# Kernel tuning notes

Hardware: AMD Instinct MI355X
Metric: run time of the kernel (lower is better)

Reference implementation:

```python
import jax, jax.numpy as jnp
import numpy as np


def setup_inputs() -> dict:
    key = jax.random.key(0)
    kx, ks = jax.random.split(key)
    X = jax.random.normal(kx, (8, 4096, 16), dtype=jnp.float32)
    # nn.Parameter(torch.rand(1) + 1.0)
    sigma = jax.random.uniform(ks, (1,), dtype=jnp.float32) + 1.0
    return {"X": X, "sigma": sigma}


def reference(X, sigma):
    sq = jnp.sum(X * X, axis=-1)                       # [B, N]
    inner = jnp.einsum('bnf,bmf->bnm', X, X)           # [B, N, N]
    sqdist = sq[:, :, None] + sq[:, None, :] - 2.0 * inner
    sqdist = jnp.maximum(sqdist, 0.0)                  # guard tiny negatives
    gaussian = jnp.exp(-sqdist / sigma[0])             # [B, N, N]
    # original _softmax: exp(gaussian) / sum over dim 2 == softmax over axis 2
    return jax.nn.softmax(gaussian, axis=2)
```

## Files before the change

### kernel.cpp

```cpp
#include <hip/hip_runtime.h>


constexpr int Bn  = 8;
constexpr int N   = 4096;
constexpr int F   = 16;
constexpr int TN  = 4;
constexpr int BLK = 512;
constexpr int WPB = BLK / 64;
constexpr int ITERS = N / (BLK * 4);

__global__ __launch_bounds__(256)
void pack_kernel(const float* __restrict__ X, float* __restrict__ Xt) {
    const int b = blockIdx.y;
    const int m = blockIdx.x * 256 + threadIdx.x;
    const float4* src = (const float4*)(X + ((size_t)b * N + m) * F);
    const float4 v0 = src[0], v1 = src[1], v2 = src[2], v3 = src[3];
    const float x[F] = {v0.x, v0.y, v0.z, v0.w, v1.x, v1.y, v1.z, v1.w,
                        v2.x, v2.y, v2.z, v2.w, v3.x, v3.y, v3.z, v3.w};
    float* dst = Xt + (size_t)b * F * N + m;
    #pragma unroll
    for (int f = 0; f < F; ++f) dst[(size_t)f * N] = x[f];
}

__device__ __forceinline__ float dot4(float4 a, float4 b) {
    return fmaf(a.x, b.x, fmaf(a.y, b.y, fmaf(a.z, b.z, a.w * b.w)));
}

__device__ __forceinline__ float gse(float d, float base, float nis) {
    float sqd = fmaxf(fmaf(-2.0f, d, base), 0.0f);
    return __expf(__expf(sqd * nis));
}

__global__ __launch_bounds__(BLK, 4)
void gs_main(const float* __restrict__ X, const float* __restrict__ Xt,
             const float* __restrict__ sigma_p, float* __restrict__ out) {
    __shared__ float lds_e[TN][N];
    __shared__ float red[TN][WPB];

    const int tid = threadIdx.x;
    const int b   = blockIdx.y;
    const int n0  = blockIdx.x * TN;
    const float* Xb = X + (size_t)b * N * F;

    float4 q0[TN], q1[TN], q2[TN], q3[TN];
    float  sqn[TN];
    #pragma unroll
    for (int r = 0; r < TN; ++r) {
        const float4* qp = (const float4*)(Xb + (size_t)(n0 + r) * F);
        q0[r] = qp[0]; q1[r] = qp[1]; q2[r] = qp[2]; q3[r] = qp[3];
        sqn[r] = dot4(q0[r], q0[r]) + dot4(q1[r], q1[r])
               + dot4(q2[r], q2[r]) + dot4(q3[r], q3[r]);
    }
    const float nis = -1.0f / sigma_p[0];

    const float4* Xt4 = (const float4*)(Xt + (size_t)b * F * N);

    float sum[TN] = {0.f, 0.f, 0.f, 0.f};

    #pragma unroll
    for (int it = 0; it < ITERS; ++it) {
        const int c4 = it * BLK + tid;

        float4 d[TN];
        #pragma unroll
        for (int r = 0; r < TN; ++r) d[r] = make_float4(0.f, 0.f, 0.f, 0.f);
        float4 sq = make_float4(0.f, 0.f, 0.f, 0.f);

        #pragma unroll
        for (int f4 = 0; f4 < F / 4; ++f4) {
            float4 v[4];
            #pragma unroll
            for (int j = 0; j < 4; ++j)
                v[j] = Xt4[(size_t)(f4 * 4 + j) * (N / 4) + c4];
            #pragma unroll
            for (int j = 0; j < 4; ++j) {
                const float4 w = v[j];
                sq.x = fmaf(w.x, w.x, sq.x);
                sq.y = fmaf(w.y, w.y, sq.y);
                sq.z = fmaf(w.z, w.z, sq.z);
                sq.w = fmaf(w.w, w.w, sq.w);
                #pragma unroll
                for (int r = 0; r < TN; ++r) {
                    const float4 qr = (f4 == 0) ? ((j == 0) ? q0[r] : (j == 1) ? q1[r] : (j == 2) ? q2[r] : q3[r])
                                                : ((j == 0) ? q0[r] : (j == 1) ? q1[r] : (j == 2) ? q2[r] : q3[r]);
                    float qf = (f4 == 0) ? 0.f : 0.f;
                    (void)qr; (void)qf;
                }
            }
        }

        #pragma unroll
        for (int r = 0; r < TN; ++r) d[r] = make_float4(0.f, 0.f, 0.f, 0.f);
        sq = make_float4(0.f, 0.f, 0.f, 0.f);

        #pragma unroll
        for (int fb = 0; fb < 4; ++fb) {
            float4 v0 = Xt4[(size_t)(fb * 4 + 0) * (N / 4) + c4];
            float4 v1 = Xt4[(size_t)(fb * 4 + 1) * (N / 4) + c4];
            float4 v2 = Xt4[(size_t)(fb * 4 + 2) * (N / 4) + c4];
            float4 v3 = Xt4[(size_t)(fb * 4 + 3) * (N / 4) + c4];

            #pragma unroll
            for (int k = 0; k < 4; ++k) {
                const float4 w = (k == 0) ? v0 : (k == 1) ? v1 : (k == 2) ? v2 : v3;
                sq.x = fmaf(w.x, w.x, sq.x);
                sq.y = fmaf(w.y, w.y, sq.y);
                sq.z = fmaf(w.z, w.z, sq.z);
                sq.w = fmaf(w.w, w.w, sq.w);
                #pragma unroll
                for (int r = 0; r < TN; ++r) {
                    const float4 qb = (fb == 0) ? q0[r] : (fb == 1) ? q1[r]
                                    : (fb == 2) ? q2[r] : q3[r];
                    const float qf = (k == 0) ? qb.x : (k == 1) ? qb.y
                                   : (k == 2) ? qb.z : qb.w;
                    d[r].x = fmaf(qf, w.x, d[r].x);
                    d[r].y = fmaf(qf, w.y, d[r].y);
                    d[r].z = fmaf(qf, w.z, d[r].z);
                    d[r].w = fmaf(qf, w.w, d[r].w);
                }
            }
        }

        #pragma unroll
        for (int r = 0; r < TN; ++r) {
            float4 e;
            e.x = gse(d[r].x, sqn[r] + sq.x, nis);
            e.y = gse(d[r].y, sqn[r] + sq.y, nis);
            e.z = gse(d[r].z, sqn[r] + sq.z, nis);
            e.w = gse(d[r].w, sqn[r] + sq.w, nis);
            ((float4*)lds_e[r])[c4] = e;
            sum[r] += (e.x + e.y) + (e.z + e.w);
        }
    }

    #pragma unroll
    for (int r = 0; r < TN; ++r) {
        float s = sum[r];
        #pragma unroll
        for (int off = 32; off > 0; off >>= 1) s += __shfl_down(s, off, 64);
        if ((tid & 63) == 0) red[r][tid >> 6] = s;
    }
    __syncthreads();

    float inv[TN];
    #pragma unroll
    for (int r = 0; r < TN; ++r) {
        float t = 0.f;
        #pragma unroll
        for (int w = 0; w < WPB; ++w) t += red[r][w];
        inv[r] = 1.0f / t;
    }

    float* outb = out + ((size_t)b * N + n0) * (size_t)N;
    #pragma unroll
    for (int r = 0; r < TN; ++r) {
        #pragma unroll
        for (int it = 0; it < ITERS; ++it) {
            const int c4 = it * BLK + tid;
            float4 v = ((const float4*)lds_e[r])[c4];
            v.x *= inv[r]; v.y *= inv[r]; v.z *= inv[r]; v.w *= inv[r];
            ((float4*)(outb + (size_t)r * N))[c4] = v;
        }
    }
}

extern "C" void kernel_launch(void* const* d_in, const int* in_sizes, int n_in,
                              void* d_out, int out_size, void* d_ws, size_t ws_size,
                              hipStream_t stream) {
    const float* X     = (const float*)d_in[0];
    const float* sigma = (const float*)d_in[1];
    float* out         = (float*)d_out;
    float* Xt          = (float*)d_ws;

    pack_kernel<<<dim3(N / 256, Bn), 256, 0, stream>>>(X, Xt);
    gs_main<<<dim3(N / TN, Bn), BLK, 0, stream>>>(X, Xt, sigma, out);
}
```

Baseline: 589.2 us.

## Split softmax into sum pass and recompute-and-write pass without LDS staging

```diff
diff --git a/kernel.cpp b/kernel.cpp
--- a/kernel.cpp
+++ b/kernel.cpp
@@ -5,9 +5,9 @@
 constexpr int N   = 4096;
 constexpr int F   = 16;
 constexpr int TN  = 4;
-constexpr int BLK = 512;
+constexpr int BLK = 256;
 constexpr int WPB = BLK / 64;
-constexpr int ITERS = N / (BLK * 4);
+constexpr int GROUPS = (N / 4) / BLK;
 
 __global__ __launch_bounds__(256)
 void pack_kernel(const float* __restrict__ X, float* __restrict__ Xt) {
@@ -31,10 +31,11 @@
     return __expf(__expf(sqd * nis));
 }
 
+template <bool WRITE>
 __global__ __launch_bounds__(BLK, 4)
-void gs_main(const float* __restrict__ X, const float* __restrict__ Xt,
-             const float* __restrict__ sigma_p, float* __restrict__ out) {
-    __shared__ float lds_e[TN][N];
+void gs_pass(const float* __restrict__ X, const float* __restrict__ Xt,
+             const float* __restrict__ sigma_p, float* __restrict__ invsum,
+             float* __restrict__ out) {
     __shared__ float red[TN][WPB];
 
     const int tid = threadIdx.x;
@@ -53,13 +54,18 @@
     }
     const float nis = -1.0f / sigma_p[0];
 
+    float inv[TN];
+    if (WRITE) {
+        #pragma unroll
+        for (int r = 0; r < TN; ++r) inv[r] = invsum[(size_t)b * N + n0 + r];
+    }
+
     const float4* Xt4 = (const float4*)(Xt + (size_t)b * F * N);
-
-    float sum[TN] = {0.f, 0.f, 0.f, 0.f};
+    float sums[TN] = {0.f, 0.f, 0.f, 0.f};
 
     #pragma unroll
-    for (int it = 0; it < ITERS; ++it) {
-        const int c4 = it * BLK + tid;
+    for (int g = 0; g < GROUPS; ++g) {
+        const int c4 = g * BLK + tid;
 
         float4 d[TN];
         #pragma unroll
@@ -67,34 +73,7 @@
         float4 sq = make_float4(0.f, 0.f, 0.f, 0.f);
 
         #pragma unroll
-        for (int f4 = 0; f4 < F / 4; ++f4) {
-            float4 v[4];
-            #pragma unroll
-            for (int j = 0; j < 4; ++j)
-                v[j] = Xt4[(size_t)(f4 * 4 + j) * (N / 4) + c4];
-            #pragma unroll
-            for (int j = 0; j < 4; ++j) {
-                const float4 w = v[j];
-                sq.x = fmaf(w.x, w.x, sq.x);
-                sq.y = fmaf(w.y, w.y, sq.y);
-                sq.z = fmaf(w.z, w.z, sq.z);
-                sq.w = fmaf(w.w, w.w, sq.w);
-                #pragma unroll
-                for (int r = 0; r < TN; ++r) {
-                    const float4 qr = (f4 == 0) ? ((j == 0) ? q0[r] : (j == 1) ? q1[r] : (j == 2) ? q2[r] : q3[r])
-                                                : ((j == 0) ? q0[r] : (j == 1) ? q1[r] : (j == 2) ? q2[r] : q3[r]);
-                    float qf = (f4 == 0) ? 0.f : 0.f;
-                    (void)qr; (void)qf;
-                }
-            }
-        }
-
-        #pragma unroll
-        for (int r = 0; r < TN; ++r) d[r] = make_float4(0.f, 0.f, 0.f, 0.f);
-        sq = make_float4(0.f, 0.f, 0.f, 0.f);
-
-        #pragma unroll
-        for (int fb = 0; fb < 4; ++fb) {
+        for (int fb = 0; fb < F / 4; ++fb) {
             float4 v0 = Xt4[(size_t)(fb * 4 + 0) * (N / 4) + c4];
             float4 v1 = Xt4[(size_t)(fb * 4 + 1) * (N / 4) + c4];
             float4 v2 = Xt4[(size_t)(fb * 4 + 2) * (N / 4) + c4];
@@ -128,38 +107,30 @@
             e.y = gse(d[r].y, sqn[r] + sq.y, nis);
             e.z = gse(d[r].z, sqn[r] + sq.z, nis);
             e.w = gse(d[r].w, sqn[r] + sq.w, nis);
-            ((float4*)lds_e[r])[c4] = e;
-            sum[r] += (e.x + e.y) + (e.z + e.w);
+            if (WRITE) {
+                float4 o = make_float4(e.x * inv[r], e.y * inv[r],
+                                       e.z * inv[r], e.w * inv[r]);
+                ((float4*)(out + ((size_t)b * N + n0 + r) * N))[c4] = o;
+            } else {
+                sums[r] += (e.x + e.y) + (e.z + e.w);
+            }
         }
     }
 
-    #pragma unroll
-    for (int r = 0; r < TN; ++r) {
-        float s = sum[r];
+    if (!WRITE) {
         #pragma unroll
-        for (int off = 32; off > 0; off >>= 1) s += __shfl_down(s, off, 64);
-        if ((tid & 63) == 0) red[r][tid >> 6] = s;
-    }
-    __syncthreads();
-
-    float inv[TN];
-    #pragma unroll
-    for (int r = 0; r < TN; ++r) {
-        float t = 0.f;
-        #pragma unroll
-        for (int w = 0; w < WPB; ++w) t += red[r][w];
-        inv[r] = 1.0f / t;
-    }
-
-    float* outb = out + ((size_t)b * N + n0) * (size_t)N;
-    #pragma unroll
-    for (int r = 0; r < TN; ++r) {
-        #pragma unroll
-        for (int it = 0; it < ITERS; ++it) {
-            const int c4 = it * BLK + tid;
-            float4 v = ((const float4*)lds_e[r])[c4];
-            v.x *= inv[r]; v.y *= inv[r]; v.z *= inv[r]; v.w *= inv[r];
-            ((float4*)(outb + (size_t)r * N))[c4] = v;
+        for (int r = 0; r < TN; ++r) {
+            float s = sums[r];
+            #pragma unroll
+            for (int off = 32; off > 0; off >>= 1) s += __shfl_down(s, off, 64);
+            if ((tid & 63) == 0) red[r][tid >> 6] = s;
+        }
+        __syncthreads();
+        if (tid < TN) {
+            float t = 0.f;
+            #pragma unroll
+            for (int w = 0; w < WPB; ++w) t += red[tid][w];
+            invsum[(size_t)b * N + n0 + tid] = 1.0f / t;
         }
     }
 }
@@ -171,7 +142,9 @@
     const float* sigma = (const float*)d_in[1];
     float* out         = (float*)d_out;
     float* Xt          = (float*)d_ws;
+    float* invsum      = (float*)d_ws + (size_t)Bn * F * N;
 
     pack_kernel<<<dim3(N / 256, Bn), 256, 0, stream>>>(X, Xt);
-    gs_main<<<dim3(N / TN, Bn), BLK, 0, stream>>>(X, Xt, sigma, out);
+    gs_pass<false><<<dim3(N / TN, Bn), BLK, 0, stream>>>(X, Xt, sigma, invsum, out);
+    gs_pass<true ><<<dim3(N / TN, Bn), BLK, 0, stream>>>(X, Xt, sigma, invsum, out);
 }
```

Result: slower. 2.004 ms (+240.1%).
